# Performance work log

Measured on AMD Instinct MI355X. Metric: run time of the kernel, lower is better.

The kernel has to match this reference:

```python
import jax, jax.numpy as jnp
import numpy as np

T, OBS, H, NOBJ = 32768, 256, 512, 4


def _xavier(key, shape):
    fan_in, fan_out = shape[0], shape[1]
    lim = jnp.sqrt(6.0 / (fan_in + fan_out)).astype(jnp.float32)
    return jax.random.uniform(key, shape, jnp.float32, -lim, lim)


def setup_inputs() -> dict:
    key = jax.random.key(0)
    ks = jax.random.split(key, 16)
    # weights stored as [in, out] so y = x @ W (same math as nn.Linear with W.T)
    return {
        "x": jax.random.normal(ks[0], (T, OBS), jnp.float32),
        "W_in0": _xavier(ks[1], (OBS, H)),
        "W_B0": _xavier(ks[2], (OBS, H)),
        "W_C0": _xavier(ks[3], (OBS, H)),
        "W_d0": _xavier(ks[4], (OBS, H)),
        "A_log0": jax.random.normal(ks[5], (H,), jnp.float32),
        "W_in1": _xavier(ks[6], (H, H)),
        "W_B1": _xavier(ks[7], (H, H)),
        "W_C1": _xavier(ks[8], (H, H)),
        "W_d1": _xavier(ks[9], (H, H)),
        "A_log1": jax.random.normal(ks[10], (H,), jnp.float32),
        "W_out": _xavier(ks[11], (H, NOBJ)),
        "b_out": jnp.zeros((NOBJ,), jnp.float32),
        "W_skip": _xavier(ks[12], (OBS, NOBJ)),
    }


def _mamba_layer(x, W_in, W_B, W_C, W_d, A_log):
    # x: [T, D_in] -> [T, H]
    x_state = x @ W_in           # [T, H]
    B = x @ W_B                  # [T, H]
    C = x @ W_C                  # [T, H]
    delta = jax.nn.sigmoid(x @ W_d)  # [T, H]
    A = -jnp.exp(A_log)          # [H]
    A_bar = jnp.exp(delta * A)   # [T, H], in (0, 1)
    Bx = B * x_state             # [T, H]

    def step(h, inp):
        a_t, bx_t = inp
        h = a_t * h + bx_t
        return h, h

    h0 = jnp.zeros((x_state.shape[-1],), x_state.dtype)
    _, h_seq = jax.lax.scan(step, h0, (A_bar, Bx))  # [T, H]
    return C * h_seq


def reference(x, W_in0, W_B0, W_C0, W_d0, A_log0,
              W_in1, W_B1, W_C1, W_d1, A_log1,
              W_out, b_out, W_skip):
    skip = x
    y = _mamba_layer(x, W_in0, W_B0, W_C0, W_d0, A_log0)
    y = _mamba_layer(y, W_in1, W_B1, W_C1, W_d1, A_log1)
    out = y @ W_out + b_out + skip @ W_skip  # [T, NOBJ]
    return out
```

## Files before the change

kernel.cpp:

```cpp
#include <hip/hip_runtime.h>

typedef __attribute__((ext_vector_type(8))) short short8;
typedef __attribute__((ext_vector_type(4))) float floatx4;

#define T_SIZE 32768
#define OBS    256
#define H      512
#define NC     1024
#define CHUNK  32
#define NGRP   64
#define GCH    16

__device__ __forceinline__ unsigned short f2bf(float f){
    union { float f; unsigned u; } v; v.f = f;
    unsigned u = v.u;
    u += 0x7FFFu + ((u >> 16) & 1u);
    return (unsigned short)(u >> 16);
}
__device__ __forceinline__ float bf2f(unsigned short u){
    union { unsigned u; float f; } v; v.u = ((unsigned)u) << 16; return v.f;
}

#define GLOAD_LDS16(g, l) \
    __builtin_amdgcn_global_load_lds((const __attribute__((address_space(1))) unsigned*)(g), \
                                     (__attribute__((address_space(3))) unsigned*)(l), 16, 0, 0)

__global__ void prep_kernel(const float* __restrict__ x, unsigned short* __restrict__ xb,
                            const float* __restrict__ A0W0, const float* __restrict__ A0W1,
                            const float* __restrict__ A0W2, const float* __restrict__ A0W3,
                            unsigned short* __restrict__ Wt0,
                            const float* __restrict__ A1W0, const float* __restrict__ A1W1,
                            const float* __restrict__ A1W2, const float* __restrict__ A1W3,
                            unsigned short* __restrict__ Wt1){
    const int b = blockIdx.x;
    const int tid = threadIdx.x;
    if (b < 8192){
        int i = b * 256 + tid;
        float4 v = ((const float4*)x)[i];
        ushort4 o;
        o.x = f2bf(v.x); o.y = f2bf(v.y); o.z = f2bf(v.z); o.w = f2bf(v.w);
        ((ushort4*)xb)[i] = o;
    } else if (b < 10240){
        const int K = OBS, KH = OBS * H;
        int idx = (b - 8192) * 256 + tid;
        int s   = idx / KH;
        int rem = idx - s * KH;
        int h = rem >> 8;
        int k = rem & 255;
        const float* W = (s == 0) ? A0W0 : (s == 1) ? A0W1 : (s == 2) ? A0W2 : A0W3;
        int bb = h >> 4, hh = h & 15;
        Wt0[(size_t)((bb * 4 + s) * 16 + hh) * K + k] = f2bf(W[(size_t)k * H + h]);
    } else {
        const int K = H, KH = H * H;
        int idx = (b - 10240) * 256 + tid;
        int s   = idx / KH;
        int rem = idx - s * KH;
        int h = rem >> 9;
        int k = rem & 511;
        const float* W = (s == 0) ? A1W0 : (s == 1) ? A1W1 : (s == 2) ? A1W2 : A1W3;
        int bb = h >> 4, hh = h & 15;
        Wt1[(size_t)((bb * 4 + s) * 16 + hh) * K + k] = f2bf(W[(size_t)k * H + h]);
    }
}

template<int K>
__global__ __launch_bounds__(256, 3) void gemm_layer_kernel(
    const unsigned short* __restrict__ xb,
    const unsigned short* __restrict__ wt,
    const float* __restrict__ A_log,
    unsigned short* __restrict__ ylT, unsigned short* __restrict__ wT,
    float* __restrict__ Pbuf, float* __restrict__ Hbuf)
{
    __shared__ unsigned short SM[3][8192];

    const int tid  = threadIdx.x;
    const int wave = tid >> 6;
    const int lane = tid & 63;
    const int ml   = lane & 15;
    const int quad = lane >> 4;
    const int wm   = wave & 1;
    const int wn   = wave >> 1;

    const int flat = blockIdx.y * 16 + blockIdx.x;
    const int xcd  = flat & 7;
    const int j    = flat >> 3;
    const int nb   = j & 15;
    const int mb   = (j >> 4) * 8 + xcd;
    const int m0   = mb * 128;

    const int srow = tid >> 2;
    const int sel  = (((tid & 3) ^ ((tid >> 3) & 3))) * 8;
    const int swz  = (ml >> 1) & 3;

    const unsigned short* pa0 = xb + (size_t)(m0 + srow) * K + sel;
    const unsigned short* pa1 = pa0 + (size_t)64 * K;
    const unsigned short* pb0 = wt + (size_t)(nb * 128 + srow) * K + sel;
    const unsigned short* pb1 = pb0 + (size_t)64 * K;

    const int ldsA0 = (wave * 64 + 0  ) * 8;
    const int ldsA1 = (wave * 64 + 256) * 8;

    const int rbaseA = (wm * 64 + ml) * 32 + (quad ^ swz) * 8;
    const int rbaseB = (wn * 64 + ml) * 32 + (quad ^ swz) * 8;

    floatx4 acc[4][4];
    #pragma unroll
    for (int i = 0; i < 4; i++)
        #pragma unroll
        for (int jj = 0; jj < 4; jj++)
            acc[i][jj] = (floatx4)(0.0f);

    constexpr int NK = K >> 5;

#define STAGE(kt_) { const int b_ = (kt_) % 3; const int ko_ = (kt_) * 32; \
        GLOAD_LDS16(pa0 + ko_, &SM[b_][ldsA0]); \
        GLOAD_LDS16(pa1 + ko_, &SM[b_][ldsA1]); \
        GLOAD_LDS16(pb0 + ko_, &SM[b_][4096 + ldsA0]); \
        GLOAD_LDS16(pb1 + ko_, &SM[b_][4096 + ldsA1]); }

    STAGE(0); STAGE(1);
    asm volatile("s_waitcnt vmcnt(4)" ::: "memory");
    __builtin_amdgcn_s_barrier();
    __builtin_amdgcn_sched_barrier(0);

    #pragma unroll
    for (int kk = 0; kk < NK; ++kk){
        const int cur = kk % 3;

        if (kk + 2 < NK) STAGE(kk + 2);

        short8 av[4], bv[4];
        #pragma unroll
        for (int i = 0; i < 4; i++)
            av[i] = *(const short8*)(&SM[cur][0] + rbaseA + i * 16 * 32);
        #pragma unroll
        for (int jj = 0; jj < 4; jj++)
            bv[jj] = *(const short8*)(&SM[cur][4096] + rbaseB + jj * 16 * 32);

        __builtin_amdgcn_s_setprio(1);
        #pragma unroll
        for (int i = 0; i < 4; i++)
            #pragma unroll
            for (int jj = 0; jj < 4; jj++)
                acc[i][jj] = __builtin_amdgcn_mfma_f32_16x16x32_bf16(av[i], bv[jj], acc[i][jj], 0, 0, 0);
        __builtin_amdgcn_s_setprio(0);

        if (kk + 1 < NK){
            if (kk + 2 < NK) { asm volatile("s_waitcnt vmcnt(4)" ::: "memory"); }
            else             { asm volatile("s_waitcnt vmcnt(0)" ::: "memory"); }
            __builtin_amdgcn_s_barrier();
            __builtin_amdgcn_sched_barrier(0);
        }
    }
    __syncthreads();

#undef STAGE

    unsigned short* SMe = &SM[0][0];
    float2* segbuf = (float2*)(SMe + 12288);
    const int col = wn * 16 + ml;
    const int h   = nb * 32 + col;
    const float Aneg = -expf(A_log[h]);

    float va[4][4], vb[4][4], vc[4][4];
    #pragma unroll
    for (int i = 0; i < 4; i++){
        float p = 1.0f, hh = 0.0f;
        #pragma unroll
        for (int r = 0; r < 4; r++){
            float dv = acc[i][3][r];
            float delta = 1.0f / (1.0f + __expf(-dv));
            float a  = __expf(delta * Aneg);
            float bx = acc[i][1][r] * acc[i][0][r];
            va[i][r] = a; vb[i][r] = bx; vc[i][r] = acc[i][2][r];
            hh = fmaf(a, hh, bx);
            p *= a;
        }
        const int ch = wm * 2 + (i >> 1);
        const int s  = (i & 1) * 4 + quad;
        segbuf[(ch * 8 + s) * 32 + col] = make_float2(p, hh);
    }
    __syncthreads();

    #pragma unroll
    for (int i = 0; i < 4; i++){
        const int ch = wm * 2 + (i >> 1);
        const int s  = (i & 1) * 4 + quad;
        float Pexc = 1.0f, Hexc = 0.0f;
        for (int sp = 0; sp < s; sp++){
            float2 ph = segbuf[(ch * 8 + sp) * 32 + col];
            Hexc = fmaf(ph.x, Hexc, ph.y);
            Pexc *= ph.x;
        }
        float hcur = Hexc, pf = Pexc;
        #pragma unroll
        for (int r = 0; r < 4; r++){
            hcur = fmaf(va[i][r], hcur, vb[i][r]);
            pf  *= va[i][r];
            int trow = wm * 64 + i * 16 + quad * 4 + r;
            SMe[        trow * 32 + col] = f2bf(vc[i][r] * hcur);
            SMe[4096 +  trow * 32 + col] = f2bf(vc[i][r] * pf);
        }
    }
    if (tid < 128){
        const int ccol = tid & 31, ch = tid >> 5;
        float P = 1.0f, Hc = 0.0f;
        #pragma unroll
        for (int s = 0; s < 8; s++){
            float2 ph = segbuf[(ch * 8 + s) * 32 + ccol];
            Hc = fmaf(ph.x, Hc, ph.y);
            P *= ph.x;
        }
        const int c = mb * 4 + ch;
        Pbuf[(size_t)c * H + nb * 32 + ccol] = P;
        Hbuf[(size_t)c * H + nb * 32 + ccol] = Hc;
    }
    __syncthreads();
    {
        const short8* s8 = (const short8*)SMe;
        #pragma unroll
        for (int arr = 0; arr < 2; arr++){
            unsigned short* bp = (arr == 0) ? ylT : wT;
            #pragma unroll
            for (int half = 0; half < 2; half++){
                int u = half * 256 + tid;
                int row = u >> 2, part = u & 3;
                *(short8*)(bp + (size_t)(m0 + row) * H + nb * 32 + part * 8) = s8[arr * 512 + u];
            }
        }
    }
}

__global__ void scan2a_kernel(const float* __restrict__ P, const float* __restrict__ Hc,
                              float* __restrict__ Pg, float* __restrict__ Hg){
    const int g  = blockIdx.x;
    const int j4 = threadIdx.x * 4;
    float4 pc = {1.f,1.f,1.f,1.f}, hc = {0.f,0.f,0.f,0.f};
    #pragma unroll
    for (int i = 0; i < GCH; i++){
        size_t o = (size_t)(g * GCH + i) * H + j4;
        float4 P4 = *(const float4*)(P + o);
        float4 H4 = *(const float4*)(Hc + o);
        hc.x = fmaf(P4.x, hc.x, H4.x); pc.x *= P4.x;
        hc.y = fmaf(P4.y, hc.y, H4.y); pc.y *= P4.y;
        hc.z = fmaf(P4.z, hc.z, H4.z); pc.z *= P4.z;
        hc.w = fmaf(P4.w, hc.w, H4.w); pc.w *= P4.w;
    }
    *(float4*)(Pg + (size_t)g * H + j4) = pc;
    *(float4*)(Hg + (size_t)g * H + j4) = hc;
}

__global__ __launch_bounds__(256) void scan3_kernel(
    const unsigned short* __restrict__ ylT, const unsigned short* __restrict__ wT,
    const float* __restrict__ P, const float* __restrict__ Hc,
    const float* __restrict__ Pg, const float* __restrict__ Hg,
    unsigned short* __restrict__ yb){
    const int c    = blockIdx.x;
    const int half = threadIdx.x >> 7;
    const int j4   = (threadIdx.x & 127) * 4;
    const int grp  = c >> 4;
    float4 h = {0.f, 0.f, 0.f, 0.f};
    for (int g = 0; g < grp; ++g){
        float4 P4 = *(const float4*)(Pg + (size_t)g * H + j4);
        float4 H4 = *(const float4*)(Hg + (size_t)g * H + j4);
        h.x = fmaf(P4.x, h.x, H4.x);
        h.y = fmaf(P4.y, h.y, H4.y);
        h.z = fmaf(P4.z, h.z, H4.z);
        h.w = fmaf(P4.w, h.w, H4.w);
    }
    for (int cc = grp << 4; cc < c; ++cc){
        float4 P4 = *(const float4*)(P + (size_t)cc * H + j4);
        float4 H4 = *(const float4*)(Hc + (size_t)cc * H + j4);
        h.x = fmaf(P4.x, h.x, H4.x);
        h.y = fmaf(P4.y, h.y, H4.y);
        h.z = fmaf(P4.z, h.z, H4.z);
        h.w = fmaf(P4.w, h.w, H4.w);
    }
    size_t off = (size_t)(c * CHUNK + half * 16) * H + j4;
    #pragma unroll 8
    for (int i = 0; i < 16; i++){
        ushort4 yl = *(const ushort4*)(ylT + off);
        ushort4 w4 = *(const ushort4*)(wT + off);
        ushort4 o;
        o.x = f2bf(fmaf(bf2f(w4.x), h.x, bf2f(yl.x)));
        o.y = f2bf(fmaf(bf2f(w4.y), h.y, bf2f(yl.y)));
        o.z = f2bf(fmaf(bf2f(w4.z), h.z, bf2f(yl.z)));
        o.w = f2bf(fmaf(bf2f(w4.w), h.w, bf2f(yl.w)));
        *(ushort4*)(yb + off) = o;
        off += H;
    }
}

__global__ __launch_bounds__(256) void scan3f_kernel(
    const unsigned short* __restrict__ ylT, const unsigned short* __restrict__ wT,
    const float* __restrict__ P, const float* __restrict__ Hc,
    const float* __restrict__ Pg, const float* __restrict__ Hg,
    const unsigned short* __restrict__ xb,
    const float* __restrict__ Wout, const float* __restrict__ bout,
    const float* __restrict__ Wskip,
    float* __restrict__ out){
    __shared__ unsigned short ystage[32 * 512];
    const int tid  = threadIdx.x;
    const int c    = blockIdx.x;
    const int half = tid >> 7;
    const int j4   = (tid & 127) * 4;
    const int grp  = c >> 4;
    float4 h = {0.f, 0.f, 0.f, 0.f};
    for (int g = 0; g < grp; ++g){
        float4 P4 = *(const float4*)(Pg + (size_t)g * H + j4);
        float4 H4 = *(const float4*)(Hg + (size_t)g * H + j4);
        h.x = fmaf(P4.x, h.x, H4.x);
        h.y = fmaf(P4.y, h.y, H4.y);
        h.z = fmaf(P4.z, h.z, H4.z);
        h.w = fmaf(P4.w, h.w, H4.w);
    }
    for (int cc = grp << 4; cc < c; ++cc){
        float4 P4 = *(const float4*)(P + (size_t)cc * H + j4);
        float4 H4 = *(const float4*)(Hc + (size_t)cc * H + j4);
        h.x = fmaf(P4.x, h.x, H4.x);
        h.y = fmaf(P4.y, h.y, H4.y);
        h.z = fmaf(P4.z, h.z, H4.z);
        h.w = fmaf(P4.w, h.w, H4.w);
    }
    size_t off = (size_t)(c * CHUNK + half * 16) * H + j4;
    #pragma unroll 8
    for (int i = 0; i < 16; i++){
        ushort4 yl = *(const ushort4*)(ylT + off);
        ushort4 w4 = *(const ushort4*)(wT + off);
        ushort4 o;
        o.x = f2bf(fmaf(bf2f(w4.x), h.x, bf2f(yl.x)));
        o.y = f2bf(fmaf(bf2f(w4.y), h.y, bf2f(yl.y)));
        o.z = f2bf(fmaf(bf2f(w4.z), h.z, bf2f(yl.z)));
        o.w = f2bf(fmaf(bf2f(w4.w), h.w, bf2f(yl.w)));
        *(ushort4*)(&ystage[(half * 16 + i) * 512 + j4]) = o;
        off += H;
    }
    __syncthreads();

    const int wave = tid >> 6;
    const int lane = tid & 63;
    const float4* W4 = (const float4*)Wout;
    const float4* S4 = (const float4*)Wskip;
    const float b0 = bout[0], b1 = bout[1], b2 = bout[2], b3 = bout[3];
    for (int rr = 0; rr < 8; ++rr){
        const int r = wave * 8 + rr;
        const int t = c * 32 + r;
        float s0 = 0.f, s1 = 0.f, s2 = 0.f, s3 = 0.f;
        #pragma unroll
        for (int k = lane; k < H; k += 64){
            float yv = bf2f(ystage[r * 512 + k]);
            float4 w = W4[k];
            s0 = fmaf(yv, w.x, s0); s1 = fmaf(yv, w.y, s1);
            s2 = fmaf(yv, w.z, s2); s3 = fmaf(yv, w.w, s3);
        }
        #pragma unroll
        for (int k = lane; k < OBS; k += 64){
            float xv = bf2f(xb[(size_t)t * OBS + k]);
            float4 w = S4[k];
            s0 = fmaf(xv, w.x, s0); s1 = fmaf(xv, w.y, s1);
            s2 = fmaf(xv, w.z, s2); s3 = fmaf(xv, w.w, s3);
        }
        #pragma unroll
        for (int o = 32; o > 0; o >>= 1){
            s0 += __shfl_down(s0, o);
            s1 += __shfl_down(s1, o);
            s2 += __shfl_down(s2, o);
            s3 += __shfl_down(s3, o);
        }
        if (lane == 0){
            out[(size_t)t * 4 + 0] = s0 + b0;
            out[(size_t)t * 4 + 1] = s1 + b1;
            out[(size_t)t * 4 + 2] = s2 + b2;
            out[(size_t)t * 4 + 3] = s3 + b3;
        }
    }
}

extern "C" void kernel_launch(void* const* d_in, const int* in_sizes, int n_in,
                              void* d_out, int out_size, void* d_ws, size_t ws_size,
                              hipStream_t stream)
{
    const float* x     = (const float*)d_in[0];
    const float* W_in0 = (const float*)d_in[1];
    const float* W_B0  = (const float*)d_in[2];
    const float* W_C0  = (const float*)d_in[3];
    const float* W_d0  = (const float*)d_in[4];
    const float* A0    = (const float*)d_in[5];
    const float* W_in1 = (const float*)d_in[6];
    const float* W_B1  = (const float*)d_in[7];
    const float* W_C1  = (const float*)d_in[8];
    const float* W_d1  = (const float*)d_in[9];
    const float* A1    = (const float*)d_in[10];
    const float* Wout  = (const float*)d_in[11];
    const float* bout  = (const float*)d_in[12];
    const float* Wskip = (const float*)d_in[13];
    float* out = (float*)d_out;

    char* ws = (char*)d_ws;
    size_t off = 0;
    auto alloc = [&](size_t bytes) -> void* {
        void* p = ws + off;
        off += (bytes + 255) & ~(size_t)255;
        return p;
    };
    unsigned short* xb  = (unsigned short*)alloc((size_t)T_SIZE * OBS * 2);
    unsigned short* yb  = (unsigned short*)alloc((size_t)T_SIZE * H * 2);
    unsigned short* Wt0 = (unsigned short*)alloc((size_t)4 * H * OBS * 2);
    unsigned short* Wt1 = (unsigned short*)alloc((size_t)4 * H * H * 2);
    unsigned short* ylT = (unsigned short*)alloc((size_t)T_SIZE * H * 2);
    unsigned short* wT  = (unsigned short*)alloc((size_t)T_SIZE * H * 2);
    float* Pbuf = (float*)alloc((size_t)NC * H * 4);
    float* Hbuf = (float*)alloc((size_t)NC * H * 4);
    float* Pg   = (float*)alloc((size_t)NGRP * H * 4);
    float* Hg   = (float*)alloc((size_t)NGRP * H * 4);
    (void)ws_size; (void)in_sizes; (void)n_in; (void)out_size;

    prep_kernel<<<14336, 256, 0, stream>>>(x, xb,
                                           W_in0, W_B0, W_C0, W_d0, Wt0,
                                           W_in1, W_B1, W_C1, W_d1, Wt1);

    dim3 ggrid(16, 256);

    gemm_layer_kernel<OBS><<<ggrid, 256, 0, stream>>>(xb, Wt0, A0, ylT, wT, Pbuf, Hbuf);
    scan2a_kernel<<<NGRP, 128, 0, stream>>>(Pbuf, Hbuf, Pg, Hg);
    scan3_kernel<<<NC, 256, 0, stream>>>(ylT, wT, Pbuf, Hbuf, Pg, Hg, yb);

    gemm_layer_kernel<H><<<ggrid, 256, 0, stream>>>(yb, Wt1, A1, ylT, wT, Pbuf, Hbuf);
    scan2a_kernel<<<NGRP, 128, 0, stream>>>(Pbuf, Hbuf, Pg, Hg);
    scan3f_kernel<<<NC, 256, 0, stream>>>(ylT, wT, Pbuf, Hbuf, Pg, Hg,
                                          xb, Wout, bout, Wskip, out);
}
```

Before: 305.3 us.

## Precompute per-chunk carry-in states in a separate scan pass

Adds a scan2b kernel that turns group aggregates and within-group exclusive prefixes into a per-chunk carry-in state. scan3 and scan3f then load that state directly instead of each block re-scanning up to 63 group aggregates plus up to 15 chunk aggregates. This removes the redundant serial prefix work spread across 1024 blocks. In exchange it adds one kernel launch per layer, extra workspace buffers, and more global writes and reads in scan2a.

```diff
diff --git a/kernel.cpp b/kernel.cpp
--- a/kernel.cpp
+++ b/kernel.cpp
@@ -232,13 +232,16 @@
 }
 
 __global__ void scan2a_kernel(const float* __restrict__ P, const float* __restrict__ Hc,
-                              float* __restrict__ Pg, float* __restrict__ Hg){
+                              float* __restrict__ Pg, float* __restrict__ Hg,
+                              float* __restrict__ Pexc, float* __restrict__ Hexc){
     const int g  = blockIdx.x;
     const int j4 = threadIdx.x * 4;
     float4 pc = {1.f,1.f,1.f,1.f}, hc = {0.f,0.f,0.f,0.f};
     #pragma unroll
     for (int i = 0; i < GCH; i++){
         size_t o = (size_t)(g * GCH + i) * H + j4;
+        *(float4*)(Pexc + o) = pc;
+        *(float4*)(Hexc + o) = hc;
         float4 P4 = *(const float4*)(P + o);
         float4 H4 = *(const float4*)(Hc + o);
         hc.x = fmaf(P4.x, hc.x, H4.x); pc.x *= P4.x;
@@ -250,32 +253,42 @@
     *(float4*)(Hg + (size_t)g * H + j4) = hc;
 }
 
+__global__ void scan2b_kernel(const float* __restrict__ Pg, const float* __restrict__ Hg,
+                              const float* __restrict__ Pexc, const float* __restrict__ Hexc,
+                              float* __restrict__ Cc){
+    const int g  = blockIdx.x;
+    const int j4 = threadIdx.x * 4;
+    float4 cg = {0.f,0.f,0.f,0.f};
+    for (int gg = 0; gg < g; ++gg){
+        float4 P4 = *(const float4*)(Pg + (size_t)gg * H + j4);
+        float4 H4 = *(const float4*)(Hg + (size_t)gg * H + j4);
+        cg.x = fmaf(P4.x, cg.x, H4.x);
+        cg.y = fmaf(P4.y, cg.y, H4.y);
+        cg.z = fmaf(P4.z, cg.z, H4.z);
+        cg.w = fmaf(P4.w, cg.w, H4.w);
+    }
+    #pragma unroll
+    for (int i = 0; i < GCH; i++){
+        size_t o = (size_t)(g * GCH + i) * H + j4;
+        float4 pe = *(const float4*)(Pexc + o);
+        float4 he = *(const float4*)(Hexc + o);
+        float4 cc;
+        cc.x = fmaf(pe.x, cg.x, he.x);
+        cc.y = fmaf(pe.y, cg.y, he.y);
+        cc.z = fmaf(pe.z, cg.z, he.z);
+        cc.w = fmaf(pe.w, cg.w, he.w);
+        *(float4*)(Cc + o) = cc;
+    }
+}
+
 __global__ __launch_bounds__(256) void scan3_kernel(
     const unsigned short* __restrict__ ylT, const unsigned short* __restrict__ wT,
-    const float* __restrict__ P, const float* __restrict__ Hc,
-    const float* __restrict__ Pg, const float* __restrict__ Hg,
+    const float* __restrict__ Cc,
     unsigned short* __restrict__ yb){
     const int c    = blockIdx.x;
     const int half = threadIdx.x >> 7;
     const int j4   = (threadIdx.x & 127) * 4;
-    const int grp  = c >> 4;
-    float4 h = {0.f, 0.f, 0.f, 0.f};
-    for (int g = 0; g < grp; ++g){
-        float4 P4 = *(const float4*)(Pg + (size_t)g * H + j4);
-        float4 H4 = *(const float4*)(Hg + (size_t)g * H + j4);
-        h.x = fmaf(P4.x, h.x, H4.x);
-        h.y = fmaf(P4.y, h.y, H4.y);
-        h.z = fmaf(P4.z, h.z, H4.z);
-        h.w = fmaf(P4.w, h.w, H4.w);
-    }
-    for (int cc = grp << 4; cc < c; ++cc){
-        float4 P4 = *(const float4*)(P + (size_t)cc * H + j4);
-        float4 H4 = *(const float4*)(Hc + (size_t)cc * H + j4);
-        h.x = fmaf(P4.x, h.x, H4.x);
-        h.y = fmaf(P4.y, h.y, H4.y);
-        h.z = fmaf(P4.z, h.z, H4.z);
-        h.w = fmaf(P4.w, h.w, H4.w);
-    }
+    float4 h = *(const float4*)(Cc + (size_t)c * H + j4);
     size_t off = (size_t)(c * CHUNK + half * 16) * H + j4;
     #pragma unroll 8
     for (int i = 0; i < 16; i++){
@@ -293,8 +306,7 @@
 
 __global__ __launch_bounds__(256) void scan3f_kernel(
     const unsigned short* __restrict__ ylT, const unsigned short* __restrict__ wT,
-    const float* __restrict__ P, const float* __restrict__ Hc,
-    const float* __restrict__ Pg, const float* __restrict__ Hg,
+    const float* __restrict__ Cc,
     const unsigned short* __restrict__ xb,
     const float* __restrict__ Wout, const float* __restrict__ bout,
     const float* __restrict__ Wskip,
@@ -304,24 +316,7 @@
     const int c    = blockIdx.x;
     const int half = tid >> 7;
     const int j4   = (tid & 127) * 4;
-    const int grp  = c >> 4;
-    float4 h = {0.f, 0.f, 0.f, 0.f};
-    for (int g = 0; g < grp; ++g){
-        float4 P4 = *(const float4*)(Pg + (size_t)g * H + j4);
-        float4 H4 = *(const float4*)(Hg + (size_t)g * H + j4);
-        h.x = fmaf(P4.x, h.x, H4.x);
-        h.y = fmaf(P4.y, h.y, H4.y);
-        h.z = fmaf(P4.z, h.z, H4.z);
-        h.w = fmaf(P4.w, h.w, H4.w);
-    }
-    for (int cc = grp << 4; cc < c; ++cc){
-        float4 P4 = *(const float4*)(P + (size_t)cc * H + j4);
-        float4 H4 = *(const float4*)(Hc + (size_t)cc * H + j4);
-        h.x = fmaf(P4.x, h.x, H4.x);
-        h.y = fmaf(P4.y, h.y, H4.y);
-        h.z = fmaf(P4.z, h.z, H4.z);
-        h.w = fmaf(P4.w, h.w, H4.w);
-    }
+    float4 h = *(const float4*)(Cc + (size_t)c * H + j4);
     size_t off = (size_t)(c * CHUNK + half * 16) * H + j4;
     #pragma unroll 8
     for (int i = 0; i < 16; i++){
@@ -411,6 +406,9 @@
     unsigned short* wT  = (unsigned short*)alloc((size_t)T_SIZE * H * 2);
     float* Pbuf = (float*)alloc((size_t)NC * H * 4);
     float* Hbuf = (float*)alloc((size_t)NC * H * 4);
+    float* Pexc = (float*)alloc((size_t)NC * H * 4);
+    float* Hexc = (float*)alloc((size_t)NC * H * 4);
+    float* Cc   = (float*)alloc((size_t)NC * H * 4);
     float* Pg   = (float*)alloc((size_t)NGRP * H * 4);
     float* Hg   = (float*)alloc((size_t)NGRP * H * 4);
     (void)ws_size; (void)in_sizes; (void)n_in; (void)out_size;
@@ -422,11 +420,13 @@
     dim3 ggrid(16, 256);
 
     gemm_layer_kernel<OBS><<<ggrid, 256, 0, stream>>>(xb, Wt0, A0, ylT, wT, Pbuf, Hbuf);
-    scan2a_kernel<<<NGRP, 128, 0, stream>>>(Pbuf, Hbuf, Pg, Hg);
-    scan3_kernel<<<NC, 256, 0, stream>>>(ylT, wT, Pbuf, Hbuf, Pg, Hg, yb);
+    scan2a_kernel<<<NGRP, 128, 0, stream>>>(Pbuf, Hbuf, Pg, Hg, Pexc, Hexc);
+    scan2b_kernel<<<NGRP, 128, 0, stream>>>(Pg, Hg, Pexc, Hexc, Cc);
+    scan3_kernel<<<NC, 256, 0, stream>>>(ylT, wT, Cc, yb);
 
     gemm_layer_kernel<H><<<ggrid, 256, 0, stream>>>(yb, Wt1, A1, ylT, wT, Pbuf, Hbuf);
-    scan2a_kernel<<<NGRP, 128, 0, stream>>>(Pbuf, Hbuf, Pg, Hg);
-    scan3f_kernel<<<NC, 256, 0, stream>>>(ylT, wT, Pbuf, Hbuf, Pg, Hg,
+    scan2a_kernel<<<NGRP, 128, 0, stream>>>(Pbuf, Hbuf, Pg, Hg, Pexc, Hexc);
+    scan2b_kernel<<<NGRP, 128, 0, stream>>>(Pg, Hg, Pexc, Hexc, Cc);
+    scan3f_kernel<<<NC, 256, 0, stream>>>(ylT, wT, Cc,
                                           xb, Wout, bout, Wskip, out);
 }
```

Measured after the change: 326.5 us. +6.9%, slower.
